# Kernel tuning notes

Measured on AMD Instinct MI355X. Metric: run time of the kernel, lower is better.

## Reference

```python
import jax, jax.numpy as jnp
import numpy as np

HIDDEN = 1024
NUM_EXPERTS = 16
TOP_K = 2
I_TEXT = 512
I_VISION = 256
NUM_SHARED = 2
NORM_MIN = 1e-12


def _sparse_moe(x, router_w, bias, gate_up, down):
    """One Ernie4_5_VLMoeSparseMoeBlock applied to flat tokens x: [T, H].

    router_w: [E, H], bias: [E] (e_score_correction_bias),
    gate_up: [E, H, 2I], down: [E, I, H].
    Returns (y [T, H], router_logits [T, E]).
    """
    T = x.shape[0]
    # fp32 router (torch runs it with autocast disabled in float32)
    logits = x @ router_w.T                                  # [T, E]
    probs = jax.nn.softmax(logits, axis=-1)
    # top-k on bias-corrected probs, but gather the *uncorrected* probs
    _, sel = jax.lax.top_k(probs + bias[None, :], TOP_K)     # [T, k]
    w = jnp.take_along_axis(probs, sel, axis=1)              # [T, k]
    w = w / jnp.maximum(jnp.sum(w, axis=-1, keepdims=True), NORM_MIN)
    # sparse combine matrix [T, E] with k nonzeros per row
    combine = jnp.zeros((T, NUM_EXPERTS), x.dtype).at[
        jnp.arange(T)[:, None], sel].add(w)
    # batched per-expert gated-SiLU MLP (dense dispatch reference)
    gu = jnp.einsum('th,ehi->eti', x, gate_up)               # [E, T, 2I]
    g, u = jnp.split(gu, 2, axis=-1)
    h = jnp.einsum('eti,eih->eth', jax.nn.silu(g) * u, down)  # [E, T, H]
    y = jnp.einsum('te,eth->th', combine, h)                 # [T, H]
    return y, logits


def setup_inputs() -> dict:
    key = jax.random.key(0)
    ks = jax.random.split(key, 16)
    s = 0.02
    B, S = 1, 1024
    return {
        'hidden_states': jax.random.normal(ks[0], (B, S, HIDDEN), jnp.float32),
        'moe_mm_token_type_ids': jax.random.randint(ks[1], (B, S), 0, 2).astype(jnp.int32),
        'text_router_weight': s * jax.random.normal(ks[2], (NUM_EXPERTS, HIDDEN), jnp.float32),
        'text_bias': s * jax.random.normal(ks[3], (NUM_EXPERTS,), jnp.float32),
        'text_gate_up': s * jax.random.normal(ks[4], (NUM_EXPERTS, HIDDEN, 2 * I_TEXT), jnp.float32),
        'text_down': s * jax.random.normal(ks[5], (NUM_EXPERTS, I_TEXT, HIDDEN), jnp.float32),
        'vision_router_weight': s * jax.random.normal(ks[6], (NUM_EXPERTS, HIDDEN), jnp.float32),
        'vision_bias': s * jax.random.normal(ks[7], (NUM_EXPERTS,), jnp.float32),
        'vision_gate_up': s * jax.random.normal(ks[8], (NUM_EXPERTS, HIDDEN, 2 * I_VISION), jnp.float32),
        'vision_down': s * jax.random.normal(ks[9], (NUM_EXPERTS, I_VISION, HIDDEN), jnp.float32),
        'shared_gate': s * jax.random.normal(ks[10], (HIDDEN, NUM_SHARED * I_TEXT), jnp.float32),
        'shared_up': s * jax.random.normal(ks[11], (HIDDEN, NUM_SHARED * I_TEXT), jnp.float32),
        'shared_down': s * jax.random.normal(ks[12], (NUM_SHARED * I_TEXT, HIDDEN), jnp.float32),
    }


def reference(hidden_states, moe_mm_token_type_ids,
              text_router_weight, text_bias, text_gate_up, text_down,
              vision_router_weight, vision_bias, vision_gate_up, vision_down,
              shared_gate, shared_up, shared_down):
    B, S, H = hidden_states.shape
    x = hidden_states.reshape(-1, H)                         # [T, H]
    # shared experts MLP (gated SiLU) on all tokens
    shared = (jax.nn.silu(x @ shared_gate) * (x @ shared_up)) @ shared_down
    # modality-isolated MoEs; each is pointwise-per-token, so running both on
    # all tokens and selecting with the mask is math-equivalent to the
    # boolean-mask dispatch in the torch code (jit-friendly, no dynamic shapes)
    y_text, lg_text = _sparse_moe(x, text_router_weight, text_bias, text_gate_up, text_down)
    y_vis, lg_vis = _sparse_moe(x, vision_router_weight, vision_bias, vision_gate_up, vision_down)
    is_vision = (moe_mm_token_type_ids.reshape(-1) != 0)[:, None]  # [T, 1]
    final = jnp.where(is_vision, y_vis, y_text) + shared
    router_logits = jnp.where(is_vision, lg_vis, lg_text)    # [T, E]
    return final.reshape(B, S, H), router_logits
```

## Files before the change

kernel.cpp:

```cpp
#include <hip/hip_runtime.h>
#include <math.h>

#define TOK  1024
#define HID  1024
#define NEXP 16

typedef __attribute__((ext_vector_type(8))) short bf16x8;
typedef __attribute__((ext_vector_type(4))) float f32x4;

#define SW_GUT 0u
#define SW_GUV 16777216u
#define SW_DNT 25165824u
#define SW_DNV 33554432u
#define SW_SG  37748736u
#define SW_SU  38797312u
#define SW_SD  39845888u
#define SW_ELEMS 40894464ull
#define WS_SMALL 6554624ull
#define WS_FAST (WS_SMALL + SW_ELEMS * 2ull)

__device__ __forceinline__ unsigned pack2(float f0, float f1) {
    union { float f; unsigned u; } a, b; a.f = f0; b.f = f1;
    return __builtin_amdgcn_perm(b.u + 0x8000u, a.u + 0x8000u, 0x07060302u);
}
__device__ __forceinline__ unsigned short f2bf(float f) {
    union { float f; unsigned u; } v; v.f = f;
    return (unsigned short)((v.u + 0x8000u) >> 16);
}

__global__ void k_init(float* __restrict__ out, int* __restrict__ counts) {
    size_t i = (size_t)blockIdx.x * blockDim.x + threadIdx.x;
    ((float4*)out)[i] = make_float4(0.f, 0.f, 0.f, 0.f);
    if (blockIdx.x == 0 && threadIdx.x < 32) counts[threadIdx.x] = 0;
}

__global__ __launch_bounds__(64)
void k_router(const float* __restrict__ x, const int* __restrict__ tt,
              const float* __restrict__ rw_t, const float* __restrict__ b_t,
              const float* __restrict__ rw_v, const float* __restrict__ b_v,
              float* __restrict__ out_logits,
              int* __restrict__ counts, int* __restrict__ lists,
              float* __restrict__ wlist, unsigned short* __restrict__ Xbf)
{
    const int t = blockIdx.x;
    const int lane = threadIdx.x;
    const bool vis = (tt[t] != 0);
    const float* rw   = vis ? rw_v : rw_t;
    const float* bias = vis ? b_v  : b_t;
    const float* xr = x + (size_t)t * HID;

#pragma unroll
    for (int jj = 0; jj < 2; ++jj) {
        int j0 = jj * 512 + lane * 8;
        float4 lo = *(const float4*)(xr + j0);
        float4 hi = *(const float4*)(xr + j0 + 4);
        union { bf16x8 v; unsigned d[4]; } u;
        u.d[0] = pack2(lo.x, lo.y); u.d[1] = pack2(lo.z, lo.w);
        u.d[2] = pack2(hi.x, hi.y); u.d[3] = pack2(hi.z, hi.w);
        *(bf16x8*)(Xbf + (size_t)t * HID + j0) = u.v;
    }

    float acc[NEXP];
#pragma unroll
    for (int e = 0; e < NEXP; ++e) acc[e] = 0.f;
    for (int j = 0; j < HID; j += 64) {
        const float xv = xr[j + lane];
#pragma unroll
        for (int e = 0; e < NEXP; ++e)
            acc[e] = fmaf(xv, rw[(size_t)e * HID + j + lane], acc[e]);
    }
#pragma unroll
    for (int e = 0; e < NEXP; ++e) {
        float v = acc[e];
#pragma unroll
        for (int off = 32; off; off >>= 1) v += __shfl_xor(v, off);
        acc[e] = v;
    }
    if (lane < NEXP) out_logits[(size_t)t * NEXP + lane] = acc[lane];

    if (lane == 0) {
        float mx = acc[0];
#pragma unroll
        for (int e = 1; e < NEXP; ++e) mx = fmaxf(mx, acc[e]);
        float p[NEXP], s = 0.f;
#pragma unroll
        for (int e = 0; e < NEXP; ++e) { p[e] = expf(acc[e] - mx); s += p[e]; }
        const float inv = 1.f / s;
#pragma unroll
        for (int e = 0; e < NEXP; ++e) p[e] *= inv;

        int s1 = 0; float v1 = p[0] + bias[0];
#pragma unroll
        for (int e = 1; e < NEXP; ++e) {
            float c = p[e] + bias[e];
            if (c > v1) { v1 = c; s1 = e; }
        }
        int s2 = -1; float v2 = -1e30f;
#pragma unroll
        for (int e = 0; e < NEXP; ++e) {
            if (e == s1) continue;
            float c = p[e] + bias[e];
            if (c > v2) { v2 = c; s2 = e; }
        }
        float w1 = p[s1], w2 = p[s2];
        float sw = fmaxf(w1 + w2, 1e-12f);
        w1 /= sw; w2 /= sw;

        const int base = vis ? NEXP : 0;
        int pos1 = atomicAdd(&counts[base + s1], 1);
        lists[(base + s1) * TOK + pos1] = t * 2 + 0;
        wlist[(base + s1) * TOK + pos1] = w1;
        int pos2 = atomicAdd(&counts[base + s2], 1);
        lists[(base + s2) * TOK + pos2] = t * 2 + 1;
        wlist[(base + s2) * TOK + pos2] = w2;
    }
}

__global__ __launch_bounds__(256)
void k_conv(const float* __restrict__ gut, const float* __restrict__ guv,
            const float* __restrict__ dnt, const float* __restrict__ dnv,
            const float* __restrict__ sg, const float* __restrict__ su,
            const float* __restrict__ sd, unsigned short* __restrict__ sw)
{
    __shared__ float ls[32 * 258];
    const int bid = blockIdx.x;
    const float* src; unsigned short* dst; int K, N, c, p;
    if (bid < 2048)      { int i = bid;        int e = i >> 7, r = i & 127; c = r >> 2; p = r & 3; K = 1024; N = 1024; src = gut + (size_t)e * 1048576; dst = sw + SW_GUT + (size_t)e * 1048576; }
    else if (bid < 3072) { int i = bid - 2048; int e = i >> 6, r = i & 63;  c = r >> 1; p = r & 1; K = 1024; N = 512;  src = guv + (size_t)e * 524288;  dst = sw + SW_GUV + (size_t)e * 524288; }
    else if (bid < 4096) { int i = bid - 3072; int e = i >> 6, r = i & 63;  c = r >> 2; p = r & 3; K = 512;  N = 1024; src = dnt + (size_t)e * 524288;  dst = sw + SW_DNT + (size_t)e * 524288; }
    else if (bid < 4608) { int i = bid - 4096; int e = i >> 5, r = i & 31;  c = r >> 2; p = r & 3; K = 256;  N = 1024; src = dnv + (size_t)e * 262144;  dst = sw + SW_DNV + (size_t)e * 262144; }
    else if (bid < 4736) { int i = bid - 4608; c = i >> 2; p = i & 3; K = 1024; N = 1024; src = sg; dst = sw + SW_SG; }
    else if (bid < 4864) { int i = bid - 4736; c = i >> 2; p = i & 3; K = 1024; N = 1024; src = su; dst = sw + SW_SU; }
    else                 { int i = bid - 4864; c = i >> 2; p = i & 3; K = 1024; N = 1024; src = sd; dst = sw + SW_SD; }

    const int k0 = c * 32, n0 = p * 256;
    const int tid = threadIdx.x;
#pragma unroll
    for (int i = 0; i < 8; ++i) {
        int u = tid + i * 256;
        int row = u >> 6, c4 = u & 63;
        float4 v = *(const float4*)(src + (size_t)(k0 + row) * N + n0 + c4 * 4);
        float* lp = &ls[row * 258 + c4 * 4];
        lp[0] = v.x; lp[1] = v.y; lp[2] = v.z; lp[3] = v.w;
    }
    __syncthreads();
    const int KC = K >> 5;
#pragma unroll
    for (int i = 0; i < 4; ++i) {
        int u = tid + i * 256;
        int tt = u >> 6, l = u & 63;
        int q = l >> 4, lm = l & 15;
        int col = tt * 16 + lm;
        unsigned d0 = pack2(ls[(q * 8 + 0) * 258 + col], ls[(q * 8 + 1) * 258 + col]);
        unsigned d1 = pack2(ls[(q * 8 + 2) * 258 + col], ls[(q * 8 + 3) * 258 + col]);
        unsigned d2 = pack2(ls[(q * 8 + 4) * 258 + col], ls[(q * 8 + 5) * 258 + col]);
        unsigned d3 = pack2(ls[(q * 8 + 6) * 258 + col], ls[(q * 8 + 7) * 258 + col]);
        size_t off = ((size_t)((p * 16 + tt) * KC + c) * 64 + l) * 8;
        *(uint4*)(dst + off) = make_uint4(d0, d1, d2, d3);
    }
}

__global__ __launch_bounds__(256)
void k_gu2(const unsigned short* __restrict__ Xbf, const unsigned short* __restrict__ sw,
           const int* __restrict__ counts, const int* __restrict__ lists,
           unsigned short* __restrict__ hbuf, unsigned short* __restrict__ hsh)
{
    const int z = blockIdx.z;
    int M, I, utile0;
    const unsigned short *gbase, *ubase;
    if (z == 32)      { M = TOK;       I = 1024; gbase = sw + SW_SG; ubase = sw + SW_SU; utile0 = 0; }
    else if (z < 16)  { M = counts[z]; I = 512;  gbase = ubase = sw + SW_GUT + (size_t)z * 1048576; utile0 = 32; }
    else              { M = counts[z]; I = 256;  gbase = ubase = sw + SW_GUV + (size_t)(z - 16) * 524288; utile0 = 16; }
    const int xI = blockIdx.x * 64, m0 = blockIdx.y * 64;
    if (xI >= I || m0 >= M) return;

    __shared__ int s_aid[64];
    const int tid = threadIdx.x;
    if (tid < 64) {
        int r = m0 + tid;
        s_aid[tid] = (z == 32) ? r : ((r < M) ? lists[z * TOK + r] : -1);
    }
    __syncthreads();

    const int w = tid >> 6, lane = tid & 63;
    const int lm = lane & 15, q = lane >> 4;

    const unsigned short* arow[4];
#pragma unroll
    for (int s = 0; s < 4; ++s) {
        int aid = s_aid[s * 16 + lm];
        int tr = (z == 32) ? aid : (aid < 0 ? 0 : (aid >> 1));
        arow[s] = Xbf + (size_t)tr * HID;
    }
    const int tg = (xI >> 4) + w;
    const int tu = utile0 + (xI >> 4) + w;
    const unsigned short* pg = gbase + (size_t)tg * 32 * 512 + lane * 8;
    const unsigned short* pu = ubase + (size_t)tu * 32 * 512 + lane * 8;
    const int ko = q * 8;

    f32x4 accG[4] = {}, accU[4] = {};
    bf16x8 Bg[4], Bu[4], Af[4][4];
#pragma unroll
    for (int p = 0; p < 4; ++p) {
        Bg[p] = *(const bf16x8*)(pg + p * 512);
        Bu[p] = *(const bf16x8*)(pu + p * 512);
        const int kg0 = p * 32 + ko;
#pragma unroll
        for (int s = 0; s < 4; ++s) Af[p][s] = *(const bf16x8*)(arow[s] + kg0);
    }
    for (int cc = 0; cc < 32; cc += 4) {
#pragma unroll
        for (int p = 0; p < 4; ++p) {
            const int c = cc + p;
#pragma unroll
            for (int s = 0; s < 4; ++s) {
                accG[s] = __builtin_amdgcn_mfma_f32_16x16x32_bf16(Af[p][s], Bg[p], accG[s], 0, 0, 0);
                accU[s] = __builtin_amdgcn_mfma_f32_16x16x32_bf16(Af[p][s], Bu[p], accU[s], 0, 0, 0);
            }
            int cp = c + 4; if (cp > 31) cp = 31;
            Bg[p] = *(const bf16x8*)(pg + cp * 512);
            Bu[p] = *(const bf16x8*)(pu + cp * 512);
            const int kgp = cp * 32 + ko;
#pragma unroll
            for (int s = 0; s < 4; ++s) Af[p][s] = *(const bf16x8*)(arow[s] + kgp);
        }
    }

    const int i = xI + w * 16 + lm;
#pragma unroll
    for (int s = 0; s < 4; ++s)
#pragma unroll
        for (int r = 0; r < 4; ++r) {
            int row = s * 16 + q * 4 + r;
            int aid = s_aid[row];
            if (aid < 0) continue;
            float g = accG[s][r], uu = accU[s][r];
            float h = g / (1.f + __expf(-g)) * uu;
            if (z == 32) hsh[(size_t)aid * 1024 + i] = f2bf(h);
            else         hbuf[(size_t)aid * 512 + i] = f2bf(h);
        }
}

__global__ __launch_bounds__(256)
void k_down2(const unsigned short* __restrict__ hbuf, const unsigned short* __restrict__ hsh,
             const unsigned short* __restrict__ sw,
             const int* __restrict__ counts, const int* __restrict__ lists,
             const float* __restrict__ wlist, float* __restrict__ out)
{
    const int z = blockIdx.z;
    int M, K;
    const unsigned short* base;
    if (z == 32)     { M = TOK;       K = 1024; base = sw + SW_SD; }
    else if (z < 16) { M = counts[z]; K = 512;  base = sw + SW_DNT + (size_t)z * 524288; }
    else             { M = counts[z]; K = 256;  base = sw + SW_DNV + (size_t)(z - 16) * 262144; }
    const int n0 = blockIdx.x * 64, m0 = blockIdx.y * 64;
    if (m0 >= M) return;

    __shared__ int s_aid[64];
    __shared__ float s_w[64];
    const int tid = threadIdx.x;
    if (tid < 64) {
        int r = m0 + tid;
        if (z == 32)    { s_aid[tid] = r; s_w[tid] = 1.f; }
        else if (r < M) { s_aid[tid] = lists[z * TOK + r]; s_w[tid] = wlist[z * TOK + r]; }
        else            { s_aid[tid] = -1; s_w[tid] = 0.f; }
    }
    __syncthreads();

    const int w = tid >> 6, lane = tid & 63;
    const int lm = lane & 15, q = lane >> 4;

    const unsigned short* hrow[4];
#pragma unroll
    for (int s = 0; s < 4; ++s) {
        int aid = s_aid[s * 16 + lm];
        hrow[s] = (z == 32) ? (hsh + (size_t)aid * 1024)
                            : (hbuf + (size_t)(aid < 0 ? 0 : aid) * 512);
    }
    const int KC = K >> 5;
    const int t = (n0 >> 4) + w;
    const unsigned short* pb = base + (size_t)t * KC * 512 + lane * 8;
    const int ko = q * 8;

    f32x4 acc[4] = {};
    bf16x8 Bt[4], Af[4][4];
#pragma unroll
    for (int p = 0; p < 4; ++p) {
        Bt[p] = *(const bf16x8*)(pb + p * 512);
        const int kg0 = p * 32 + ko;
#pragma unroll
        for (int s = 0; s < 4; ++s) Af[p][s] = *(const bf16x8*)(hrow[s] + kg0);
    }
    const int last = KC - 1;
    for (int cc = 0; cc < KC; cc += 4) {
#pragma unroll
        for (int p = 0; p < 4; ++p) {
            const int c = cc + p;
            (void)c;
#pragma unroll
            for (int s = 0; s < 4; ++s)
                acc[s] = __builtin_amdgcn_mfma_f32_16x16x32_bf16(Af[p][s], Bt[p], acc[s], 0, 0, 0);
            int cp = cc + p + 4; if (cp > last) cp = last;
            Bt[p] = *(const bf16x8*)(pb + (size_t)cp * 512);
            const int kgp = cp * 32 + ko;
#pragma unroll
            for (int s = 0; s < 4; ++s) Af[p][s] = *(const bf16x8*)(hrow[s] + kgp);
        }
    }

    const int col = n0 + w * 16 + lm;
#pragma unroll
    for (int s = 0; s < 4; ++s)
#pragma unroll
        for (int r = 0; r < 4; ++r) {
            int row = s * 16 + q * 4 + r;
            int aid = s_aid[row];
            if (aid < 0) continue;
            int tok = (z == 32) ? aid : (aid >> 1);
            atomicAdd(&out[(size_t)tok * HID + col], s_w[row] * acc[s][r]);
        }
}

__global__ __launch_bounds__(256)
void k_gu_fb(const unsigned short* __restrict__ Xbf,
             const float* __restrict__ gut, const float* __restrict__ guv,
             const float* __restrict__ sg, const float* __restrict__ su,
             const int* __restrict__ counts, const int* __restrict__ lists,
             unsigned short* __restrict__ hbuf, unsigned short* __restrict__ hsh)
{
    const int z = blockIdx.z;
    int M, I, str;
    const float *Wg, *Wu;
    if (z == 32) { M = TOK; I = 1024; str = 1024; Wg = sg; Wu = su; }
    else {
        M = counts[z];
        const int mod = z >> 4, e = z & 15;
        I = mod ? 256 : 512; str = 2 * I;
        const float* base = mod ? (guv + (size_t)e * HID * 512)
                                : (gut + (size_t)e * HID * 1024);
        Wg = base; Wu = base + I;
    }
    const int xI = blockIdx.x * 64;
    const int m0 = blockIdx.y * 64;
    if (xI >= I || m0 >= M) return;

    __shared__ float bs[8192];
    __shared__ int s_aid[64];
    const int tid = threadIdx.x;
    const int wid = tid >> 6, lane = tid & 63;
    const int lm = lane & 15, q = lane >> 4;

    if (tid < 64) {
        int r = m0 + tid;
        s_aid[tid] = (z == 32) ? r : ((r < M) ? lists[z * TOK + r] : -1);
    }
    __syncthreads();

    const unsigned short* arow[4];
#pragma unroll
    for (int s = 0; s < 4; ++s) {
        int aid = s_aid[s * 16 + lm];
        int tr = (z == 32) ? aid : (aid < 0 ? 0 : (aid >> 1));
        arow[s] = Xbf + (size_t)tr * HID;
    }
    int urow[8], uc4[8], scell[8];
#pragma unroll
    for (int r = 0; r < 8; ++r) {
        int u = r * 256 + tid;
        int k = u >> 5;
        urow[r] = k; uc4[r] = u & 31;
        scell[r] = k * 32 + ((u & 31) ^ (((k >> 3) & 1) << 2));
    }
    int fidx[2];
#pragma unroll
    for (int reg = 0; reg < 2; ++reg) {
        int c = reg * 64 + wid * 16 + lm;
        fidx[reg] = (q * 8) * 128 + (((c >> 2) ^ ((q & 1) << 2)) * 4 + (c & 3));
    }
    float4 R[8];
#pragma unroll
    for (int r = 0; r < 8; ++r) {
        int c4 = uc4[r];
        const float* gp = (c4 < 16) ? (Wg + (size_t)urow[r] * str + xI + c4 * 4)
                                    : (Wu + (size_t)urow[r] * str + xI + (c4 - 16) * 4);
        R[r] = *(const float4*)gp;
    }
    f32x4 accG[4] = {}, accU[4] = {};
    for (int kc = 0; kc < 16; ++kc) {
        if (kc) __syncthreads();
#pragma unroll
        for (int r = 0; r < 8; ++r)
            *(float4*)&bs[scell[r] * 4] = R[r];
        __syncthreads();
        bf16x8 af[2][4];
        const int kg = kc * 64 + q * 8;
#pragma unroll
        for (int s = 0; s < 4; ++s) {
            af[0][s] = *(const bf16x8*)(arow[s] + kg);
            af[1][s] = *(const bf16x8*)(arow[s] + kg + 32);
        }
        if (kc + 1 < 16) {
            const int k0 = (kc + 1) * 64;
#pragma unroll
            for (int r = 0; r < 8; ++r) {
                int c4 = uc4[r];
                const float* gp = (c4 < 16) ? (Wg + (size_t)(k0 + urow[r]) * str + xI + c4 * 4)
                                            : (Wu + (size_t)(k0 + urow[r]) * str + xI + (c4 - 16) * 4);
                R[r] = *(const float4*)gp;
            }
        }
#pragma unroll
        for (int ks2 = 0; ks2 < 2; ++ks2) {
            const int ks = ks2 * 32;
            bf16x8 bg, bu;
            {
                float b[8];
#pragma unroll
                for (int j = 0; j < 8; ++j) b[j] = bs[fidx[0] + (ks + j) * 128];
                union { bf16x8 v; unsigned d[4]; } u;
                u.d[0] = pack2(b[0], b[1]); u.d[1] = pack2(b[2], b[3]);
                u.d[2] = pack2(b[4], b[5]); u.d[3] = pack2(b[6], b[7]);
                bg = u.v;
            }
            {
                float b[8];
#pragma unroll
                for (int j = 0; j < 8; ++j) b[j] = bs[fidx[1] + (ks + j) * 128];
                union { bf16x8 v; unsigned d[4]; } u;
                u.d[0] = pack2(b[0], b[1]); u.d[1] = pack2(b[2], b[3]);
                u.d[2] = pack2(b[4], b[5]); u.d[3] = pack2(b[6], b[7]);
                bu = u.v;
            }
#pragma unroll
            for (int s = 0; s < 4; ++s) {
                accG[s] = __builtin_amdgcn_mfma_f32_16x16x32_bf16(af[ks2][s], bg, accG[s], 0, 0, 0);
                accU[s] = __builtin_amdgcn_mfma_f32_16x16x32_bf16(af[ks2][s], bu, accU[s], 0, 0, 0);
            }
        }
    }
    const int i = xI + wid * 16 + lm;
#pragma unroll
    for (int s = 0; s < 4; ++s)
#pragma unroll
        for (int r = 0; r < 4; ++r) {
            int row = s * 16 + q * 4 + r;
            int aid = s_aid[row];
            if (aid < 0) continue;
            float g = accG[s][r], uu = accU[s][r];
            float h = g / (1.f + __expf(-g)) * uu;
            if (z == 32) hsh[(size_t)aid * 1024 + i] = f2bf(h);
            else         hbuf[(size_t)aid * 512 + i] = f2bf(h);
        }
}

__global__ __launch_bounds__(256)
void k_down_fb(const unsigned short* __restrict__ hbuf, const unsigned short* __restrict__ hsh,
               const float* __restrict__ dnt, const float* __restrict__ dnv,
               const float* __restrict__ sd,
               const int* __restrict__ counts, const int* __restrict__ lists,
               const float* __restrict__ wlist, float* __restrict__ out)
{
    const int z = blockIdx.z;
    int M, K;
    const float* W;
    if (z == 32) { M = TOK; K = 1024; W = sd; }
    else {
        M = counts[z];
        const int mod = z >> 4, e = z & 15;
        K = mod ? 256 : 512;
        W = mod ? (dnv + (size_t)e * 256 * 1024) : (dnt + (size_t)e * 512 * 1024);
    }
    const int n0 = blockIdx.x * 128;
    const int m0 = blockIdx.y * 64;
    if (m0 >= M) return;

    __shared__ float bs[8192];
    __shared__ int s_aid[64];
    __shared__ float s_w[64];
    const int tid = threadIdx.x;
    const int wid = tid >> 6, lane = tid & 63;
    const int lm = lane & 15, q = lane >> 4;

    if (tid < 64) {
        int r = m0 + tid;
        if (z == 32)    { s_aid[tid] = r; s_w[tid] = 1.f; }
        else if (r < M) { s_aid[tid] = lists[z * TOK + r]; s_w[tid] = wlist[z * TOK + r]; }
        else            { s_aid[tid] = -1; s_w[tid] = 0.f; }
    }
    __syncthreads();

    const unsigned short* hrow[4];
#pragma unroll
    for (int s = 0; s < 4; ++s) {
        int aid = s_aid[s * 16 + lm];
        hrow[s] = (z == 32) ? (hsh + (size_t)aid * 1024)
                            : (hbuf + (size_t)(aid < 0 ? 0 : aid) * 512);
    }
    int urow[8], uc4[8], scell[8];
#pragma unroll
    for (int r = 0; r < 8; ++r) {
        int u = r * 256 + tid;
        int k = u >> 5;
        urow[r] = k; uc4[r] = u & 31;
        scell[r] = k * 32 + ((u & 31) ^ (((k >> 3) & 1) << 2));
    }
    int fidx[2];
#pragma unroll
    for (int t = 0; t < 2; ++t) {
        int c = wid * 32 + t * 16 + lm;
        fidx[t] = (q * 8) * 128 + (((c >> 2) ^ ((q & 1) << 2)) * 4 + (c & 3));
    }
    float4 R[8];
#pragma unroll
    for (int r = 0; r < 8; ++r)
        R[r] = *(const float4*)(W + (size_t)urow[r] * 1024 + n0 + uc4[r] * 4);

    f32x4 acc[4][2] = {};
    const int NC = K >> 6;
    for (int kc = 0; kc < NC; ++kc) {
        if (kc) __syncthreads();
#pragma unroll
        for (int r = 0; r < 8; ++r)
            *(float4*)&bs[scell[r] * 4] = R[r];
        __syncthreads();
        bf16x8 af[2][4];
        const int kg = kc * 64 + q * 8;
#pragma unroll
        for (int s = 0; s < 4; ++s) {
            af[0][s] = *(const bf16x8*)(hrow[s] + kg);
            af[1][s] = *(const bf16x8*)(hrow[s] + kg + 32);
        }
        if (kc + 1 < NC) {
            const int k0 = (kc + 1) * 64;
#pragma unroll
            for (int r = 0; r < 8; ++r)
                R[r] = *(const float4*)(W + (size_t)(k0 + urow[r]) * 1024 + n0 + uc4[r] * 4);
        }
#pragma unroll
        for (int ks2 = 0; ks2 < 2; ++ks2) {
            const int ks = ks2 * 32;
            bf16x8 bt[2];
#pragma unroll
            for (int t = 0; t < 2; ++t) {
                float b[8];
#pragma unroll
                for (int j = 0; j < 8; ++j) b[j] = bs[fidx[t] + (ks + j) * 128];
                union { bf16x8 v; unsigned d[4]; } u;
                u.d[0] = pack2(b[0], b[1]); u.d[1] = pack2(b[2], b[3]);
                u.d[2] = pack2(b[4], b[5]); u.d[3] = pack2(b[6], b[7]);
                bt[t] = u.v;
            }
#pragma unroll
            for (int s = 0; s < 4; ++s)
#pragma unroll
                for (int t = 0; t < 2; ++t)
                    acc[s][t] = __builtin_amdgcn_mfma_f32_16x16x32_bf16(af[ks2][s], bt[t], acc[s][t], 0, 0, 0);
        }
    }
#pragma unroll
    for (int s = 0; s < 4; ++s)
#pragma unroll
        for (int r = 0; r < 4; ++r) {
            int row = s * 16 + q * 4 + r;
            int aid = s_aid[row];
            if (aid < 0) continue;
            int tok = (z == 32) ? aid : (aid >> 1);
            float w = s_w[row];
#pragma unroll
            for (int t = 0; t < 2; ++t) {
                int col = n0 + wid * 32 + t * 16 + lm;
                atomicAdd(&out[(size_t)tok * HID + col], w * acc[s][t][r]);
            }
        }
}

extern "C" void kernel_launch(void* const* d_in, const int* in_sizes, int n_in,
                              void* d_out, int out_size, void* d_ws, size_t ws_size,
                              hipStream_t stream)
{
    const float* x    = (const float*)d_in[0];
    const int*   tt   = (const int*)d_in[1];
    const float* rw_t = (const float*)d_in[2];
    const float* b_t  = (const float*)d_in[3];
    const float* gu_t = (const float*)d_in[4];
    const float* dn_t = (const float*)d_in[5];
    const float* rw_v = (const float*)d_in[6];
    const float* b_v  = (const float*)d_in[7];
    const float* gu_v = (const float*)d_in[8];
    const float* dn_v = (const float*)d_in[9];
    const float* sg   = (const float*)d_in[10];
    const float* su   = (const float*)d_in[11];
    const float* sd   = (const float*)d_in[12];
    float* out = (float*)d_out;
    float* out_logits = out + (size_t)TOK * HID;

    char* ws = (char*)d_ws;
    int*   counts = (int*)ws;
    int*   lists  = (int*)(ws + 1024);
    float* wlist  = (float*)(ws + 1024 + 32 * TOK * 4);
    unsigned short* hbuf = (unsigned short*)(ws + 1024 + 64 * TOK * 4);
    unsigned short* hsh  = hbuf + (size_t)2048 * 512;
    unsigned short* Xbf  = hsh + (size_t)1024 * 1024;
    unsigned short* swz  = Xbf + (size_t)1024 * 1024;

    hipLaunchKernelGGL(k_init, dim3(1024), dim3(256), 0, stream, out, counts);
    hipLaunchKernelGGL(k_router, dim3(TOK), dim3(64), 0, stream,
                       x, tt, rw_t, b_t, rw_v, b_v, out_logits, counts, lists, wlist, Xbf);
    if (ws_size >= WS_FAST) {
        hipLaunchKernelGGL(k_conv, dim3(4992), dim3(256), 0, stream,
                           gu_t, gu_v, dn_t, dn_v, sg, su, sd, swz);
        hipLaunchKernelGGL(k_gu2, dim3(16, 16, 33), dim3(256), 0, stream,
                           Xbf, swz, counts, lists, hbuf, hsh);
        hipLaunchKernelGGL(k_down2, dim3(16, 16, 33), dim3(256), 0, stream,
                           hbuf, hsh, swz, counts, lists, wlist, out);
    } else {
        hipLaunchKernelGGL(k_gu_fb, dim3(16, 16, 33), dim3(256), 0, stream,
                           Xbf, gu_t, gu_v, sg, su, counts, lists, hbuf, hsh);
        hipLaunchKernelGGL(k_down_fb, dim3(8, 16, 33), dim3(256), 0, stream,
                           hbuf, hsh, dn_t, dn_v, sd, counts, lists, wlist, out);
    }
}
```

Before: 371.9 us.

## Shrink GEMM block tiles to 64x16 with one 16x16 MFMA tile per wave

The gate-up and down expert GEMM kernels now give each wave a single 16-row by 16-column output tile, where before each wave held four 16-row slices, and the grid grows fourfold in x to match. Per-wave register use and accumulator count fall, which raises occupancy and parallelism for the small, uneven per-expert token counts. In exchange, each B-weight fragment is reused across 16 rows per wave instead of 64, so weight reads from L2/HBM grow roughly fourfold. Four times as many blocks are launched.

```diff
diff --git a/kernel.cpp b/kernel.cpp
--- a/kernel.cpp
+++ b/kernel.cpp
@@ -171,7 +171,7 @@
     if (z == 32)      { M = TOK;       I = 1024; gbase = sw + SW_SG; ubase = sw + SW_SU; utile0 = 0; }
     else if (z < 16)  { M = counts[z]; I = 512;  gbase = ubase = sw + SW_GUT + (size_t)z * 1048576; utile0 = 32; }
     else              { M = counts[z]; I = 256;  gbase = ubase = sw + SW_GUV + (size_t)(z - 16) * 524288; utile0 = 16; }
-    const int xI = blockIdx.x * 64, m0 = blockIdx.y * 64;
+    const int xI = blockIdx.x * 16, m0 = blockIdx.y * 64;
     if (xI >= I || m0 >= M) return;
 
     __shared__ int s_aid[64];
@@ -185,60 +185,47 @@
     const int w = tid >> 6, lane = tid & 63;
     const int lm = lane & 15, q = lane >> 4;
 
-    const unsigned short* arow[4];
-#pragma unroll
-    for (int s = 0; s < 4; ++s) {
-        int aid = s_aid[s * 16 + lm];
-        int tr = (z == 32) ? aid : (aid < 0 ? 0 : (aid >> 1));
-        arow[s] = Xbf + (size_t)tr * HID;
-    }
-    const int tg = (xI >> 4) + w;
-    const int tu = utile0 + (xI >> 4) + w;
+    int aidA = s_aid[w * 16 + lm];
+    int tr = (z == 32) ? aidA : (aidA < 0 ? 0 : (aidA >> 1));
+    const unsigned short* arow = Xbf + (size_t)tr * HID;
+
+    const int tg = xI >> 4;
+    const int tu = utile0 + tg;
     const unsigned short* pg = gbase + (size_t)tg * 32 * 512 + lane * 8;
     const unsigned short* pu = ubase + (size_t)tu * 32 * 512 + lane * 8;
     const int ko = q * 8;
 
-    f32x4 accG[4] = {}, accU[4] = {};
-    bf16x8 Bg[4], Bu[4], Af[4][4];
+    f32x4 accG = {}, accU = {};
+    bf16x8 Bg[4], Bu[4], Af[4];
 #pragma unroll
     for (int p = 0; p < 4; ++p) {
         Bg[p] = *(const bf16x8*)(pg + p * 512);
         Bu[p] = *(const bf16x8*)(pu + p * 512);
-        const int kg0 = p * 32 + ko;
-#pragma unroll
-        for (int s = 0; s < 4; ++s) Af[p][s] = *(const bf16x8*)(arow[s] + kg0);
+        Af[p] = *(const bf16x8*)(arow + p * 32 + ko);
     }
     for (int cc = 0; cc < 32; cc += 4) {
 #pragma unroll
         for (int p = 0; p < 4; ++p) {
-            const int c = cc + p;
-#pragma unroll
-            for (int s = 0; s < 4; ++s) {
-                accG[s] = __builtin_amdgcn_mfma_f32_16x16x32_bf16(Af[p][s], Bg[p], accG[s], 0, 0, 0);
-                accU[s] = __builtin_amdgcn_mfma_f32_16x16x32_bf16(Af[p][s], Bu[p], accU[s], 0, 0, 0);
-            }
-            int cp = c + 4; if (cp > 31) cp = 31;
+            accG = __builtin_amdgcn_mfma_f32_16x16x32_bf16(Af[p], Bg[p], accG, 0, 0, 0);
+            accU = __builtin_amdgcn_mfma_f32_16x16x32_bf16(Af[p], Bu[p], accU, 0, 0, 0);
+            int cp = cc + p + 4; if (cp > 31) cp = 31;
             Bg[p] = *(const bf16x8*)(pg + cp * 512);
             Bu[p] = *(const bf16x8*)(pu + cp * 512);
-            const int kgp = cp * 32 + ko;
-#pragma unroll
-            for (int s = 0; s < 4; ++s) Af[p][s] = *(const bf16x8*)(arow[s] + kgp);
-        }
-    }
-
-    const int i = xI + w * 16 + lm;
-#pragma unroll
-    for (int s = 0; s < 4; ++s)
-#pragma unroll
-        for (int r = 0; r < 4; ++r) {
-            int row = s * 16 + q * 4 + r;
-            int aid = s_aid[row];
-            if (aid < 0) continue;
-            float g = accG[s][r], uu = accU[s][r];
-            float h = g / (1.f + __expf(-g)) * uu;
-            if (z == 32) hsh[(size_t)aid * 1024 + i] = f2bf(h);
-            else         hbuf[(size_t)aid * 512 + i] = f2bf(h);
-        }
+            Af[p] = *(const bf16x8*)(arow + cp * 32 + ko);
+        }
+    }
+
+    const int i = xI + lm;
+#pragma unroll
+    for (int r = 0; r < 4; ++r) {
+        int row = w * 16 + q * 4 + r;
+        int aid = s_aid[row];
+        if (aid < 0) continue;
+        float g = accG[r], uu = accU[r];
+        float h = g / (1.f + __expf(-g)) * uu;
+        if (z == 32) hsh[(size_t)aid * 1024 + i] = f2bf(h);
+        else         hbuf[(size_t)aid * 512 + i] = f2bf(h);
+    }
 }
 
 __global__ __launch_bounds__(256)
@@ -253,7 +240,7 @@
     if (z == 32)     { M = TOK;       K = 1024; base = sw + SW_SD; }
     else if (z < 16) { M = counts[z]; K = 512;  base = sw + SW_DNT + (size_t)z * 524288; }
     else             { M = counts[z]; K = 256;  base = sw + SW_DNV + (size_t)(z - 16) * 262144; }
-    const int n0 = blockIdx.x * 64, m0 = blockIdx.y * 64;
+    const int n0 = blockIdx.x * 16, m0 = blockIdx.y * 64;
     if (m0 >= M) return;
 
     __shared__ int s_aid[64];
@@ -270,55 +257,42 @@
     const int w = tid >> 6, lane = tid & 63;
     const int lm = lane & 15, q = lane >> 4;
 
-    const unsigned short* hrow[4];
-#pragma unroll
-    for (int s = 0; s < 4; ++s) {
-        int aid = s_aid[s * 16 + lm];
-        hrow[s] = (z == 32) ? (hsh + (size_t)aid * 1024)
-                            : (hbuf + (size_t)(aid < 0 ? 0 : aid) * 512);
-    }
+    int aidA = s_aid[w * 16 + lm];
+    const unsigned short* hrow = (z == 32) ? (hsh + (size_t)aidA * 1024)
+                                           : (hbuf + (size_t)(aidA < 0 ? 0 : aidA) * 512);
+
     const int KC = K >> 5;
-    const int t = (n0 >> 4) + w;
+    const int t = blockIdx.x;
     const unsigned short* pb = base + (size_t)t * KC * 512 + lane * 8;
     const int ko = q * 8;
 
-    f32x4 acc[4] = {};
-    bf16x8 Bt[4], Af[4][4];
+    f32x4 acc = {};
+    bf16x8 Bt[4], Af[4];
 #pragma unroll
     for (int p = 0; p < 4; ++p) {
         Bt[p] = *(const bf16x8*)(pb + p * 512);
-        const int kg0 = p * 32 + ko;
-#pragma unroll
-        for (int s = 0; s < 4; ++s) Af[p][s] = *(const bf16x8*)(hrow[s] + kg0);
+        Af[p] = *(const bf16x8*)(hrow + p * 32 + ko);
     }
     const int last = KC - 1;
     for (int cc = 0; cc < KC; cc += 4) {
 #pragma unroll
         for (int p = 0; p < 4; ++p) {
-            const int c = cc + p;
-            (void)c;
-#pragma unroll
-            for (int s = 0; s < 4; ++s)
-                acc[s] = __builtin_amdgcn_mfma_f32_16x16x32_bf16(Af[p][s], Bt[p], acc[s], 0, 0, 0);
+            acc = __builtin_amdgcn_mfma_f32_16x16x32_bf16(Af[p], Bt[p], acc, 0, 0, 0);
             int cp = cc + p + 4; if (cp > last) cp = last;
             Bt[p] = *(const bf16x8*)(pb + (size_t)cp * 512);
-            const int kgp = cp * 32 + ko;
-#pragma unroll
-            for (int s = 0; s < 4; ++s) Af[p][s] = *(const bf16x8*)(hrow[s] + kgp);
-        }
-    }
-
-    const int col = n0 + w * 16 + lm;
-#pragma unroll
-    for (int s = 0; s < 4; ++s)
-#pragma unroll
-        for (int r = 0; r < 4; ++r) {
-            int row = s * 16 + q * 4 + r;
-            int aid = s_aid[row];
-            if (aid < 0) continue;
-            int tok = (z == 32) ? aid : (aid >> 1);
-            atomicAdd(&out[(size_t)tok * HID + col], s_w[row] * acc[s][r]);
-        }
+            Af[p] = *(const bf16x8*)(hrow + cp * 32 + ko);
+        }
+    }
+
+    const int col = n0 + lm;
+#pragma unroll
+    for (int r = 0; r < 4; ++r) {
+        int row = w * 16 + q * 4 + r;
+        int aid = s_aid[row];
+        if (aid < 0) continue;
+        int tok = (z == 32) ? aid : (aid >> 1);
+        atomicAdd(&out[(size_t)tok * HID + col], s_w[row] * acc[r]);
+    }
 }
 
 __global__ __launch_bounds__(256)
@@ -609,9 +583,9 @@
     if (ws_size >= WS_FAST) {
         hipLaunchKernelGGL(k_conv, dim3(4992), dim3(256), 0, stream,
                            gu_t, gu_v, dn_t, dn_v, sg, su, sd, swz);
-        hipLaunchKernelGGL(k_gu2, dim3(16, 16, 33), dim3(256), 0, stream,
+        hipLaunchKernelGGL(k_gu2, dim3(64, 16, 33), dim3(256), 0, stream,
                            Xbf, swz, counts, lists, hbuf, hsh);
-        hipLaunchKernelGGL(k_down2, dim3(16, 16, 33), dim3(256), 0, stream,
+        hipLaunchKernelGGL(k_down2, dim3(64, 16, 33), dim3(256), 0, stream,
                            hbuf, hsh, swz, counts, lists, wlist, out);
     } else {
         hipLaunchKernelGGL(k_gu_fb, dim3(16, 16, 33), dim3(256), 0, stream,
```

After: 333.4 us. 1.12x faster.
